# Performance work log

Measured on AMD Instinct MI355X. Metric: run time of the kernel, lower is better.

Reference implementation:

```python
import jax, jax.numpy as jnp
import numpy as np

LAYERS = 8
K = 2  # kernel size


def _causal_conv(x, w, b, dilation):
    # x: [B, C, T]; w: [Cout, Cin, K] (torch OIW layout); b: [Cout]
    pad = (K - 1) * dilation
    y = jax.lax.conv_general_dilated(
        x, w,
        window_strides=(1,),
        padding=[(pad, 0)],
        rhs_dilation=(dilation,),
        dimension_numbers=("NCH", "OIH", "NCH"),
    )
    return y + b[None, :, None]


def setup_inputs() -> dict:
    key = jax.random.key(0)
    ks = jax.random.split(key, 5)
    B, C, T = 16, 256, 4096
    scale = 1.0 / np.sqrt(C * K)
    return {
        "ys": jax.random.normal(ks[0], (B, C, T), dtype=jnp.float32),
        "filters_w": jax.random.normal(ks[1], (LAYERS, C, C, K), dtype=jnp.float32) * scale,
        "filters_b": jax.random.normal(ks[2], (LAYERS, C), dtype=jnp.float32) * scale,
        "gates_w": jax.random.normal(ks[3], (LAYERS, C, C, K), dtype=jnp.float32) * scale,
        "gates_b": jax.random.normal(ks[4], (LAYERS, C), dtype=jnp.float32) * scale,
    }


def reference(ys, filters_w, filters_b, gates_w, gates_b):
    Zs = ys
    Zout = jnp.zeros_like(ys)
    for l in range(LAYERS):
        d = 2 ** l
        F_ = jnp.tanh(_causal_conv(Zs, filters_w[l], filters_b[l], d))
        G_ = jax.nn.sigmoid(_causal_conv(Zs, gates_w[l], gates_b[l], d))
        Zs = F_ * G_
        Zout = Zout + Zs
    return Zout
```

## Files before the change

### kernel.cpp

```cpp
#include <hip/hip_runtime.h>


typedef __attribute__((ext_vector_type(8))) short s16x8;
typedef __attribute__((ext_vector_type(4))) short s16x4;
typedef __attribute__((ext_vector_type(4))) float f32x4;

#define NB 16
#define NC 256
#define NT 4096
#define TPAD 4224
#define PADT 128
#define NLAYERS 8
#define KTOT 512
#define MSTK 512

__device__ __forceinline__ short f2bf(float x) {
  union { float f; unsigned u; } v; v.f = x;
  unsigned u = v.u;
  unsigned r = (u + 0x7fffu + ((u >> 16) & 1u)) >> 16;
  return (short)r;
}
__device__ __forceinline__ float bf2f(short s) {
  union { float f; unsigned u; } v; v.u = ((unsigned)(unsigned short)s) << 16;
  return v.f;
}

__device__ __forceinline__ void async16(short* lp, const short* gp) {
  __builtin_amdgcn_global_load_lds(
      (const __attribute__((address_space(1))) unsigned int*)gp,
      (__attribute__((address_space(3))) unsigned int*)lp,
      16, 0, 0);
}


__global__ void zero_pads(short* __restrict__ base, int nbuf, size_t strideSh) {
  int idx = blockIdx.x * 256 + threadIdx.x;
  if (idx >= nbuf * NB * PADT * NC) return;
  int j = idx >> 19;
  int rem = idx & 524287;
  int b = rem >> 15;
  int r2 = rem & 32767;
  base[(size_t)j * strideSh + (size_t)b * TPAD * NC + r2] = 0;
}

__global__ void transpose_cast(const float* __restrict__ ys, short* __restrict__ X0) {
  __shared__ float tile[64][65];
  const int b = blockIdx.z, c0 = blockIdx.y * 64, t0 = blockIdx.x * 64;
  const int tid = threadIdx.x;
#pragma unroll
  for (int i = 0; i < 16; ++i) {
    int c = (tid >> 6) + i * 4;
    int t = tid & 63;
    tile[c][t] = ys[((size_t)(b * NC + c0 + c)) * NT + t0 + t];
  }
  __syncthreads();
#pragma unroll
  for (int i = 0; i < 2; ++i) {
    int q = tid + i * 256;
    int t = q >> 3, cc = (q & 7) * 8;
    s16x8 v;
#pragma unroll
    for (int j = 0; j < 8; ++j) v[j] = f2bf(tile[cc + j][t]);
    *(s16x8*)&X0[((size_t)(b * TPAD + PADT + t0 + t)) * NC + c0 + cc] = v;
  }
}

__global__ void convert_w(const float* __restrict__ fw, const float* __restrict__ gw,
                          short* __restrict__ Ws) {
  int idx = blockIdx.x * 256 + threadIdx.x;
  if (idx >= NLAYERS * MSTK * KTOT) return;
  int k = idx & (KTOT - 1);
  int r = (idx >> 9) & (MSTK - 1);
  int l = idx >> 18;
  int kw = k >> 8, ci = k & 255;
  int j = r >> 5, s = (r >> 4) & 1, c16 = r & 15;
  int ch = j * 16 + c16;
  int src = ((l * NC + ch) * NC + ci) * 2 + kw;
  Ws[idx] = f2bf(s ? gw[src] : fw[src]);
}

__global__ __launch_bounds__(256, 2)
void wavenet_layer(const short* __restrict__ Xin, short* __restrict__ Xout,
                   const short* __restrict__ Wl,
                   const float* __restrict__ bia_f, const float* __restrict__ bia_g,
                   float* __restrict__ Z, const short* __restrict__ Xprev,
                   int d, int zmode, int writeX) {
  __shared__ short lds[16384];

  const int tid = threadIdx.x;
  const int wave = tid >> 6, lane = tid & 63;
  const int quad = lane >> 4, l16 = lane & 15;
  const int wm = wave >> 1, wn = wave & 1;

  int flat = blockIdx.x + 4 * (blockIdx.y + 32 * blockIdx.z);
  int swz = (flat & 7) * 256 + (flat >> 3);
  const int mt = swz & 3;
  const int ty = (swz >> 2) & 31;
  const int b  = swz >> 7;
  const int m0s = mt * 128;
  const int t0  = ty * 128;

  const short* Wm = Wl + (size_t)m0s * KTOT;
  const short* Xb = Xin + ((size_t)b * TPAD + PADT + t0) * NC;

  f32x4 acc[4][4] = {};
  const int xo = (quad ^ ((l16 >> 1) & 3)) * 8;

  auto STAGE = [&](int buf, int kk) {
    short* Ad = lds + buf * 4096;
    short* Bd = lds + 8192 + buf * 4096;
    const int kw = kk >> 3;
    const int ci0 = (kk & 7) * 32;
    const int k0 = kw * 256 + ci0;
    const int tsh = (kw == 0) ? -d : 0;
#pragma unroll
    for (int i = 0; i < 2; ++i) {
      int q = i * 256 + tid;
      int r = q >> 2;
      int kc = ((q & 3) ^ ((r >> 1) & 3)) * 8;
      async16(Ad + q * 8, Wm + r * KTOT + k0 + kc);
      async16(Bd + q * 8, Xb + (r + tsh) * NC + ci0 + kc);
    }
  };

  STAGE(0, 0);
  STAGE(1, 1);
  asm volatile("s_waitcnt vmcnt(4)" ::: "memory");
  __builtin_amdgcn_sched_barrier(0);
  __builtin_amdgcn_s_barrier();

  int cur = 0;
#pragma unroll 2
  for (int kk = 0; kk < 16; ++kk) {
    const short* Ar = lds + cur * 4096;
    const short* Br = lds + 8192 + cur * 4096;
    s16x8 bfr[4];
#pragma unroll
    for (int ni = 0; ni < 4; ++ni)
      bfr[ni] = *(const s16x8*)&Br[(wn * 64 + ni * 16 + l16) * 32 + xo];
    __builtin_amdgcn_s_setprio(1);
#pragma unroll
    for (int mi = 0; mi < 4; ++mi) {
      s16x8 af = *(const s16x8*)&Ar[(wm * 64 + mi * 16 + l16) * 32 + xo];
#pragma unroll
      for (int ni = 0; ni < 4; ++ni)
        acc[mi][ni] = __builtin_amdgcn_mfma_f32_16x16x32_bf16(af, bfr[ni], acc[mi][ni], 0, 0, 0);
    }
    __builtin_amdgcn_s_setprio(0);
    if (kk == 15) break;
    asm volatile("s_waitcnt lgkmcnt(0)" ::: "memory");
    __builtin_amdgcn_sched_barrier(0);
    __builtin_amdgcn_s_barrier();
    __builtin_amdgcn_sched_barrier(0);
    if (kk < 14) {
      STAGE(cur, kk + 2);
      asm volatile("s_waitcnt vmcnt(4)" ::: "memory");
    } else {
      asm volatile("s_waitcnt vmcnt(0)" ::: "memory");
    }
    __builtin_amdgcn_sched_barrier(0);
    __builtin_amdgcn_s_barrier();
    __builtin_amdgcn_sched_barrier(0);
    cur ^= 1;
  }
  __syncthreads();

  short* ZT = lds;

#pragma unroll
  for (int p = 0; p < 2; ++p) {
    const int cloc = (wm * 2 + p) * 16 + quad * 4;
    const int ch = mt * 64 + cloc;
    float4 bf4 = *(const float4*)&bia_f[ch];
    float4 bg4 = *(const float4*)&bia_g[ch];
    const float* bfp = (const float*)&bf4;
    const float* bgp = (const float*)&bg4;
#pragma unroll
    for (int ni = 0; ni < 4; ++ni) {
      const int tl = wn * 64 + ni * 16 + l16;
      short pk[4];
#pragma unroll
      for (int r = 0; r < 4; ++r) {
        float f = acc[2 * p][ni][r] + bfp[r];
        float g = acc[2 * p + 1][ni][r] + bgp[r];
        float ef = __expf(2.f * f);
        float th = 1.f - 2.f / (ef + 1.f);
        float sg = 1.f / (1.f + __expf(-g));
        pk[r] = f2bf(th * sg);
      }
      short* dst = &ZT[tl * 64 + ((cloc + tl * 8) & 63)];
      *(s16x4*)dst = (s16x4){pk[0], pk[1], pk[2], pk[3]};
    }
  }
  __syncthreads();
#pragma unroll
  for (int i = 0; i < 4; ++i) {
    int q = tid + i * 256;
    int t = q >> 3, cc = (q & 7) * 8;
    s16x8 v = *(const s16x8*)&ZT[t * 64 + ((cc + t * 8) & 63)];
    const size_t xoff = ((size_t)(b * TPAD + PADT + t0 + t)) * NC + mt * 64 + cc;
    if (writeX) *(s16x8*)&Xout[xoff] = v;
    if (zmode) {
      s16x8 xv = *(const s16x8*)&Xin[xoff];
      float zv[8];
#pragma unroll
      for (int j = 0; j < 8; ++j) zv[j] = bf2f(v[j]) + bf2f(xv[j]);
      if (Xprev) {
        s16x8 pv = *(const s16x8*)&Xprev[xoff];
#pragma unroll
        for (int j = 0; j < 8; ++j) zv[j] += bf2f(pv[j]);
      }
      size_t zo = ((size_t)b * NT + t0 + t) * NC + mt * 64 + cc;
      if (zmode == 2) {
        float4 a0 = *(const float4*)&Z[zo];
        float4 a1 = *(const float4*)&Z[zo + 4];
        zv[0] += a0.x; zv[1] += a0.y; zv[2] += a0.z; zv[3] += a0.w;
        zv[4] += a1.x; zv[5] += a1.y; zv[6] += a1.z; zv[7] += a1.w;
      }
      *(float4*)&Z[zo]     = make_float4(zv[0], zv[1], zv[2], zv[3]);
      *(float4*)&Z[zo + 4] = make_float4(zv[4], zv[5], zv[6], zv[7]);
    }
  }
}

__global__ void transpose_out(const float* __restrict__ src, float* __restrict__ dst) {
  __shared__ float tile[64][65];
  const int b = blockIdx.z, c0 = blockIdx.y * 64, t0 = blockIdx.x * 64;
  const int tid = threadIdx.x;
#pragma unroll
  for (int i = 0; i < 4; ++i) {
    int q = tid + i * 256;
    int t = q >> 4, c = (q & 15) * 4;
    float4 v = *(const float4*)&src[((size_t)b * NT + t0 + t) * NC + c0 + c];
    tile[t][c] = v.x; tile[t][c + 1] = v.y; tile[t][c + 2] = v.z; tile[t][c + 3] = v.w;
  }
  __syncthreads();
#pragma unroll
  for (int i = 0; i < 4; ++i) {
    int q = tid + i * 256;
    int c = q >> 4, t = (q & 15) * 4;
    float4 v = make_float4(tile[t][c], tile[t + 1][c], tile[t + 2][c], tile[t + 3][c]);
    *(float4*)&dst[((size_t)b * NC + c0 + c) * NT + t0 + t] = v;
  }
}

__global__ void copy4(const float4* __restrict__ s, float4* __restrict__ d, int n) {
  int i = blockIdx.x * 256 + threadIdx.x;
  int stride = gridDim.x * 256;
  for (; i < n; i += stride) d[i] = s[i];
}

extern "C" void kernel_launch(void* const* d_in, const int* in_sizes, int n_in,
                              void* d_out, int out_size, void* d_ws, size_t ws_size,
                              hipStream_t stream) {
  const float* ys = (const float*)d_in[0];
  const float* fw = (const float*)d_in[1];
  const float* fb = (const float*)d_in[2];
  const float* gw = (const float*)d_in[3];
  const float* gb = (const float*)d_in[4];
  float* Zout = (float*)d_out;

  char* ws = (char*)d_ws;
  const size_t xbytes = (size_t)NB * TPAD * NC * 2;
  const size_t strideSh = xbytes / 2;
  const size_t wbytes = (size_t)NLAYERS * MSTK * KTOT * 2;
  const size_t zbytes = (size_t)NB * NC * NT * 4;

  int tier;
  if (ws_size >= 3 * xbytes + wbytes + zbytes)      tier = 1;
  else if (ws_size >= 3 * xbytes + wbytes)          tier = 2;
  else                                              tier = 3;

  const int nxb = (tier <= 2) ? 3 : 2;
  short* Xbase = (short*)ws;
  short* Ws = (short*)(ws + nxb * xbytes);
  float* Zacc = (tier == 1) ? (float*)(ws + 3 * xbytes + wbytes) : Zout;

  {
    int total = nxb * NB * PADT * NC;
    hipLaunchKernelGGL(zero_pads, dim3((total + 255) / 256), dim3(256), 0, stream,
                       Xbase, nxb, strideSh);
  }
  hipLaunchKernelGGL(transpose_cast, dim3(64, 4, 16), dim3(256), 0, stream, ys, Xbase);
  hipLaunchKernelGGL(convert_w, dim3(8192), dim3(256), 0, stream, fw, gw, Ws);

  for (int l = 0; l < NLAYERS; ++l) {
    const short* Xin;
    short* Xo;
    int zmode;
    const short* Xprev = nullptr;
    if (tier <= 2) {
      Xin = Xbase + (size_t)(l % 3) * strideSh;
      Xo  = Xbase + (size_t)((l + 1) % 3) * strideSh;
      if (l == 2)      { zmode = 1; Xprev = Xbase + strideSh; }
      else if (l == 5) { zmode = 2; Xprev = Xbase + strideSh; }
      else if (l == 7) { zmode = 2; }
      else             { zmode = 0; }
    } else {
      Xin = (l & 1) ? Xbase + strideSh : Xbase;
      Xo  = (l & 1) ? Xbase : Xbase + strideSh;
      zmode = (l & 1) ? ((l == 1) ? 1 : 2) : 0;
    }
    int writeX = (l < NLAYERS - 1) ? 1 : 0;
    hipLaunchKernelGGL(wavenet_layer, dim3(4, 32, 16), dim3(256), 0, stream,
                       Xin, Xo,
                       Ws + (size_t)l * MSTK * KTOT,
                       fb + l * NC, gb + l * NC, Zacc, Xprev,
                       1 << l, zmode, writeX);
  }

  if (tier == 1) {
    hipLaunchKernelGGL(transpose_out, dim3(64, 4, 16), dim3(256), 0, stream,
                       Zacc, Zout);
  } else {
    float* tmp = (float*)ws;
    hipLaunchKernelGGL(transpose_out, dim3(64, 4, 16), dim3(256), 0, stream,
                       Zacc, tmp);
    int n4 = (int)(zbytes / 16);
    hipLaunchKernelGGL(copy4, dim3(2048), dim3(256), 0, stream,
                       (const float4*)tmp, (float4*)Zout, n4);
  }
}
```

Before: 545.6 us.

## Triple-buffer LDS k-loop and accumulate Z every four layers with four X buffers

The GEMM main loop moves from double to triple buffering in LDS. Staging of tile kk+2 is issued right after the B fragments are read, which removes one of the two barriers per iteration and lets global loads overlap the MFMA work. Separately, when workspace allows, four rotating X buffers are used so the Z accumulation epilogue runs only at layers 3 and 7, each summing two earlier activations, cutting Z read-modify-write traffic. LDS use rises from 32 KB to 48 KB per block, which may limit occupancy at the requested 2 blocks per CU.

```diff
diff --git a/kernel.cpp b/kernel.cpp
--- a/kernel.cpp
+++ b/kernel.cpp
@@ -83,9 +83,10 @@
 void wavenet_layer(const short* __restrict__ Xin, short* __restrict__ Xout,
                    const short* __restrict__ Wl,
                    const float* __restrict__ bia_f, const float* __restrict__ bia_g,
-                   float* __restrict__ Z, const short* __restrict__ Xprev,
+                   float* __restrict__ Z,
+                   const short* __restrict__ Xp1, const short* __restrict__ Xp2,
                    int d, int zmode, int writeX) {
-  __shared__ short lds[16384];
+  __shared__ short lds[24576];
 
   const int tid = threadIdx.x;
   const int wave = tid >> 6, lane = tid & 63;
@@ -108,7 +109,7 @@
 
   auto STAGE = [&](int buf, int kk) {
     short* Ad = lds + buf * 4096;
-    short* Bd = lds + 8192 + buf * 4096;
+    short* Bd = lds + 12288 + buf * 4096;
     const int kw = kk >> 3;
     const int ci0 = (kk & 7) * 32;
     const int k0 = kw * 256 + ci0;
@@ -129,15 +130,16 @@
   __builtin_amdgcn_sched_barrier(0);
   __builtin_amdgcn_s_barrier();
 
-  int cur = 0;
-#pragma unroll 2
+#pragma unroll
   for (int kk = 0; kk < 16; ++kk) {
+    const int cur = kk % 3;
     const short* Ar = lds + cur * 4096;
-    const short* Br = lds + 8192 + cur * 4096;
+    const short* Br = lds + 12288 + cur * 4096;
     s16x8 bfr[4];
 #pragma unroll
     for (int ni = 0; ni < 4; ++ni)
       bfr[ni] = *(const s16x8*)&Br[(wn * 64 + ni * 16 + l16) * 32 + xo];
+    if (kk < 14) STAGE((kk + 2) % 3, kk + 2);
     __builtin_amdgcn_s_setprio(1);
 #pragma unroll
     for (int mi = 0; mi < 4; ++mi) {
@@ -148,20 +150,11 @@
     }
     __builtin_amdgcn_s_setprio(0);
     if (kk == 15) break;
-    asm volatile("s_waitcnt lgkmcnt(0)" ::: "memory");
+    if (kk < 14) asm volatile("s_waitcnt vmcnt(4)" ::: "memory");
+    else         asm volatile("s_waitcnt vmcnt(0)" ::: "memory");
     __builtin_amdgcn_sched_barrier(0);
     __builtin_amdgcn_s_barrier();
     __builtin_amdgcn_sched_barrier(0);
-    if (kk < 14) {
-      STAGE(cur, kk + 2);
-      asm volatile("s_waitcnt vmcnt(4)" ::: "memory");
-    } else {
-      asm volatile("s_waitcnt vmcnt(0)" ::: "memory");
-    }
-    __builtin_amdgcn_sched_barrier(0);
-    __builtin_amdgcn_s_barrier();
-    __builtin_amdgcn_sched_barrier(0);
-    cur ^= 1;
   }
   __syncthreads();
 
@@ -205,8 +198,13 @@
       float zv[8];
 #pragma unroll
       for (int j = 0; j < 8; ++j) zv[j] = bf2f(v[j]) + bf2f(xv[j]);
-      if (Xprev) {
-        s16x8 pv = *(const s16x8*)&Xprev[xoff];
+      if (Xp1) {
+        s16x8 pv = *(const s16x8*)&Xp1[xoff];
+#pragma unroll
+        for (int j = 0; j < 8; ++j) zv[j] += bf2f(pv[j]);
+      }
+      if (Xp2) {
+        s16x8 pv = *(const s16x8*)&Xp2[xoff];
 #pragma unroll
         for (int j = 0; j < 8; ++j) zv[j] += bf2f(pv[j]);
       }
@@ -266,15 +264,16 @@
   const size_t wbytes = (size_t)NLAYERS * MSTK * KTOT * 2;
   const size_t zbytes = (size_t)NB * NC * NT * 4;
 
-  int tier;
-  if (ws_size >= 3 * xbytes + wbytes + zbytes)      tier = 1;
-  else if (ws_size >= 3 * xbytes + wbytes)          tier = 2;
-  else                                              tier = 3;
-
-  const int nxb = (tier <= 2) ? 3 : 2;
+  int nxb, zws;
+  if      (ws_size >= 4 * xbytes + wbytes + zbytes) { nxb = 4; zws = 1; }
+  else if (ws_size >= 3 * xbytes + wbytes + zbytes) { nxb = 3; zws = 1; }
+  else if (ws_size >= 4 * xbytes + wbytes)          { nxb = 4; zws = 0; }
+  else if (ws_size >= 3 * xbytes + wbytes)          { nxb = 3; zws = 0; }
+  else                                              { nxb = 2; zws = 0; }
+
   short* Xbase = (short*)ws;
-  short* Ws = (short*)(ws + nxb * xbytes);
-  float* Zacc = (tier == 1) ? (float*)(ws + 3 * xbytes + wbytes) : Zout;
+  short* Ws = (short*)(ws + (size_t)nxb * xbytes);
+  float* Zacc = zws ? (float*)(ws + (size_t)nxb * xbytes + wbytes) : Zout;
 
   {
     int total = nxb * NB * PADT * NC;
@@ -287,15 +286,23 @@
   for (int l = 0; l < NLAYERS; ++l) {
     const short* Xin;
     short* Xo;
-    int zmode;
-    const short* Xprev = nullptr;
-    if (tier <= 2) {
-      Xin = Xbase + (size_t)(l % 3) * strideSh;
-      Xo  = Xbase + (size_t)((l + 1) % 3) * strideSh;
-      if (l == 2)      { zmode = 1; Xprev = Xbase + strideSh; }
-      else if (l == 5) { zmode = 2; Xprev = Xbase + strideSh; }
-      else if (l == 7) { zmode = 2; }
-      else             { zmode = 0; }
+    int zmode = 0;
+    const short* Xp1 = nullptr;
+    const short* Xp2 = nullptr;
+    if (nxb >= 3) {
+      Xin = Xbase + (size_t)(l % nxb) * strideSh;
+      Xo  = Xbase + (size_t)((l + 1) % nxb) * strideSh;
+      if (nxb == 4) {
+        if (l == 3 || l == 7) {
+          zmode = (l == 3) ? 1 : 2;
+          Xp1 = Xbase + 2 * strideSh;
+          Xp2 = Xbase + 1 * strideSh;
+        }
+      } else {
+        if (l == 2)      { zmode = 1; Xp1 = Xbase + strideSh; }
+        else if (l == 5) { zmode = 2; Xp1 = Xbase + strideSh; }
+        else if (l == 7) { zmode = 2; }
+      }
     } else {
       Xin = (l & 1) ? Xbase + strideSh : Xbase;
       Xo  = (l & 1) ? Xbase : Xbase + strideSh;
@@ -305,11 +312,11 @@
     hipLaunchKernelGGL(wavenet_layer, dim3(4, 32, 16), dim3(256), 0, stream,
                        Xin, Xo,
                        Ws + (size_t)l * MSTK * KTOT,
-                       fb + l * NC, gb + l * NC, Zacc, Xprev,
+                       fb + l * NC, gb + l * NC, Zacc, Xp1, Xp2,
                        1 << l, zmode, writeX);
   }
 
-  if (tier == 1) {
+  if (zws) {
     hipLaunchKernelGGL(transpose_out, dim3(64, 4, 16), dim3(256), 0, stream,
                        Zacc, Zout);
   } else {
```

After: 584.4 us. 7.1% more time.
